# Performance work log

Hardware: AMD Instinct MI355X
Metric: run time of the kernel (lower is better)

The kernel has to match this reference:

```python
import jax, jax.numpy as jnp
import numpy as np

B, T, I, H, FUT = 16384, 50, 6, 128, 30


def setup_inputs() -> dict:
    key = jax.random.key(0)
    ks = jax.random.split(key, 10)
    bound = 1.0 / np.sqrt(H)
    u = lambda k, shape: jax.random.uniform(k, shape, jnp.float32, -bound, bound)
    return {
        "history": jax.random.normal(ks[0], (B, T, I), jnp.float32),
        # GRU weights (PyTorch layout: gates stacked [r, z, n])
        "w_ih": u(ks[1], (3 * H, I)),
        "w_hh": u(ks[2], (3 * H, H)),
        "b_ih": u(ks[3], (3 * H,)),
        "b_hh": u(ks[4], (3 * H,)),
        # MLP head: Linear(H,H) -> ReLU -> Linear(H,I)
        "w1": u(ks[5], (H, H)),
        "b1": u(ks[6], (H,)),
        "w2": u(ks[7], (I, H)),
        "b2": u(ks[8], (I,)),
    }


def _gru_cell(h, x, w_ih, w_hh, b_ih, b_hh):
    # PyTorch GRU cell: gates ordered r, z, n
    gi = x @ w_ih.T + b_ih          # (B, 3H)
    gh = h @ w_hh.T + b_hh          # (B, 3H)
    i_r, i_z, i_n = jnp.split(gi, 3, axis=-1)
    h_r, h_z, h_n = jnp.split(gh, 3, axis=-1)
    r = jax.nn.sigmoid(i_r + h_r)
    z = jax.nn.sigmoid(i_z + h_z)
    n = jnp.tanh(i_n + r * h_n)
    return (1.0 - z) * n + z * h


def reference(history, w_ih, w_hh, b_ih, b_hh, w1, b1, w2, b2):
    # --- encode history: scan GRU over time ---
    h0 = jnp.zeros((history.shape[0], H), history.dtype)

    def enc_step(h, x_t):
        return _gru_cell(h, x_t, w_ih, w_hh, b_ih, b_hh), None

    h_last, _ = jax.lax.scan(enc_step, h0, jnp.swapaxes(history, 0, 1))  # (B, H)

    def head(h):
        return jax.nn.relu(h @ w1.T + b1) @ w2.T + b2  # (B, I)

    def dec_step(carry, _):
        h, x = carry
        h = _gru_cell(h, x, w_ih, w_hh, b_ih, b_hh)
        x = head(h)
        return (h, x), x

    x0 = history[:, -1]  # (B, I)
    _, preds = jax.lax.scan(dec_step, (h_last, x0), None, length=FUT)  # (FUT, B, I)
    return jnp.swapaxes(preds, 0, 1)  # (B, FUT, I)
```

## Files before the change

kernel.cpp:

```cpp
#include <hip/hip_runtime.h>

typedef _Float16 half8 __attribute__((ext_vector_type(8)));
typedef float f32x4 __attribute__((ext_vector_type(4)));

#define ROWS 32
#define HP 136
#define HBUFSZ (ROWS * HP)
#define LOG2E 1.442695041f
#define MFMA(a, b, c) __builtin_amdgcn_mfma_f32_16x16x32_f16((a), (b), (c), 0, 0, 0)

__global__ __launch_bounds__(512, 4)
void traj_gru(const float* __restrict__ history,
              const float* __restrict__ w_ih, const float* __restrict__ w_hh,
              const float* __restrict__ b_ih, const float* __restrict__ b_hh,
              const float* __restrict__ w1, const float* __restrict__ b1,
              const float* __restrict__ w2, const float* __restrict__ b2,
              float* __restrict__ out)
{
    __shared__ __align__(16) _Float16 hbuf[2 * HBUFSZ];
    __shared__ __align__(16) _Float16 xhist[50 * ROWS * 8];
    __shared__ __align__(16) _Float16 xdec[ROWS * 8];
    __shared__ __align__(16) _Float16 a1s[ROWS * HP];
    __shared__ __align__(16) _Float16 w2f[4 * 4 * 16 * 8];

    const int tid  = threadIdx.x;
    const int wave = tid >> 6;
    const int lane = tid & 63;
    const int ln16 = lane & 15;
    const int q    = lane >> 4;
    const int rowbase = blockIdx.x * ROWS;
    const int cbase = wave * 16;

    for (int i = tid; i < 2 * HBUFSZ; i += 512) hbuf[i] = (_Float16)0;
    for (int i = tid; i < 50 * ROWS * 8; i += 512) xhist[i] = (_Float16)0;
    for (int i = tid; i < ROWS * 8; i += 512) xdec[i] = (_Float16)0;
    for (int i = tid; i < 4 * 4 * 16 * 8; i += 512) w2f[i] = (_Float16)0;
    __syncthreads();

    for (int idx = tid; idx < ROWS * 300; idx += 512) {
        int r = idx / 300, rem = idx - r * 300;
        int t = rem / 6, c = rem - t * 6;
        xhist[(t * ROWS + r) * 8 + c] = (_Float16)history[(rowbase + r) * 300 + rem];
    }
    for (int idx = tid; idx < 50 * ROWS; idx += 512)
        xhist[idx * 8 + 6] = (_Float16)1.0f;
    for (int idx = tid; idx < ROWS; idx += 512)
        xdec[idx * 8 + 6] = (_Float16)1.0f;
    for (int idx = tid; idx < 6 * 128; idx += 512) {
        int n = idx >> 7, k = idx & 127;
        int kt = k >> 5, qq = (k >> 3) & 3, j = k & 7;
        w2f[((kt * 4 + qq) * 16 + n) * 8 + j] = (_Float16)w2[n * 128 + k];
    }

    half8 Bh[3][4];
    #pragma unroll
    for (int g = 0; g < 3; ++g) {
        float sc = (g < 2) ? -LOG2E : -2.0f * LOG2E;
        #pragma unroll
        for (int kt = 0; kt < 4; ++kt) {
            int n = g * 128 + cbase + ln16;
            const float* p = w_hh + n * 128 + kt * 32 + q * 8;
            half8 v;
            #pragma unroll
            for (int j = 0; j < 8; ++j) v[j] = (_Float16)(p[j] * sc);
            Bh[g][kt] = v;
        }
    }
    half8 Bi[3];
    #pragma unroll
    for (int g = 0; g < 3; ++g) {
        float sc = (g < 2) ? -LOG2E : -2.0f * LOG2E;
        int n = g * 128 + cbase + ln16;
        half8 v;
        #pragma unroll
        for (int j = 0; j < 8; ++j) v[j] = (_Float16)0.0f;
        if (q == 0) {
            #pragma unroll
            for (int j = 0; j < 6; ++j) v[j] = (_Float16)(w_ih[n * 6 + j] * sc);
            v[6] = (_Float16)((b_ih[n] + (g < 2 ? b_hh[n] : 0.0f)) * sc);
        }
        Bi[g] = v;
    }
    const float bhn = b_hh[256 + cbase + ln16] * (-2.0f * LOG2E);
    half8 Bw1[4];
    #pragma unroll
    for (int kt = 0; kt < 4; ++kt) {
        int n = cbase + ln16;
        const float* p = w1 + n * 128 + kt * 32 + q * 8;
        half8 v;
        #pragma unroll
        for (int j = 0; j < 8; ++j) v[j] = (_Float16)p[j];
        Bw1[kt] = v;
    }
    const float b1r = b1[cbase + ln16];
    const float b2r = (ln16 < 6) ? b2[ln16] : 0.0f;

    float hp[2][4] = {};

    __syncthreads();

    auto gru_step = [&](int p, const _Float16* xp) {
        const _Float16* hb = hbuf + p * HBUFSZ;
        _Float16*       hn = hbuf + (p ^ 1) * HBUFSZ;
        #pragma unroll
        for (int mt = 0; mt < 2; ++mt) {
            const _Float16* rp = hb + (mt * 16 + ln16) * HP + q * 8;
            half8 Ax = {0,0,0,0,0,0,0,0};
            if (q == 0) Ax = *(const half8*)(xp + (mt * 16 + ln16) * 8);
            f32x4 ar = {0,0,0,0}, az = {0,0,0,0}, ah = {0,0,0,0}, an = {0,0,0,0};
            half8 Acur = *(const half8*)(rp);
            #pragma unroll
            for (int kt = 0; kt < 4; ++kt) {
                half8 Anext;
                if (kt < 3) Anext = *(const half8*)(rp + (kt + 1) * 32);
                ar = MFMA(Acur, Bh[0][kt], ar);
                az = MFMA(Acur, Bh[1][kt], az);
                ah = MFMA(Acur, Bh[2][kt], ah);
                Acur = Anext;
            }
            ar = MFMA(Ax, Bi[0], ar);
            az = MFMA(Ax, Bi[1], az);
            an = MFMA(Ax, Bi[2], an);
            _Float16* wp = hn + (mt * 16 + q * 4) * HP + cbase + ln16;
            #pragma unroll
            for (int i = 0; i < 4; ++i) {
                float r = __builtin_amdgcn_rcpf(1.0f + __builtin_amdgcn_exp2f(ar[i]));
                float z = __builtin_amdgcn_rcpf(1.0f + __builtin_amdgcn_exp2f(az[i]));
                float t = an[i] + r * (ah[i] + bhn);
                float n = 2.0f * __builtin_amdgcn_rcpf(1.0f + __builtin_amdgcn_exp2f(t)) - 1.0f;
                float h = n + z * (hp[mt][i] - n);
                hp[mt][i] = h;
                wp[i * HP] = (_Float16)h;
            }
        }
        __syncthreads();
    };

    auto head_step = [&](int f, int p) {
        const _Float16* hb = hbuf + p * HBUFSZ;
        #pragma unroll
        for (int mt = 0; mt < 2; ++mt) {
            const _Float16* rp = hb + (mt * 16 + ln16) * HP + q * 8;
            f32x4 a = {0,0,0,0};
            half8 Acur = *(const half8*)(rp);
            #pragma unroll
            for (int kt = 0; kt < 4; ++kt) {
                half8 Anext;
                if (kt < 3) Anext = *(const half8*)(rp + (kt + 1) * 32);
                a = MFMA(Acur, Bw1[kt], a);
                Acur = Anext;
            }
            _Float16* wp = a1s + (mt * 16 + q * 4) * HP + cbase + ln16;
            #pragma unroll
            for (int i = 0; i < 4; ++i) {
                float v = a[i] + b1r;
                v = v > 0.0f ? v : 0.0f;
                wp[i * HP] = (_Float16)v;
            }
        }
        __syncthreads();
        if (wave < 2) {
            f32x4 o = {0,0,0,0};
            #pragma unroll
            for (int kt = 0; kt < 4; ++kt) {
                half8 Aa = *(const half8*)&a1s[(wave * 16 + ln16) * HP + kt * 32 + q * 8];
                half8 Bw = *(const half8*)&w2f[((kt * 4 + q) * 16 + ln16) * 8];
                o = MFMA(Aa, Bw, o);
            }
            if (ln16 < 6) {
                #pragma unroll
                for (int i = 0; i < 4; ++i) {
                    int row = wave * 16 + q * 4 + i;
                    float v = o[i] + b2r;
                    out[(rowbase + row) * 180 + f * 6 + ln16] = v;
                    xdec[row * 8 + ln16] = (_Float16)v;
                }
            }
        }
        __syncthreads();
    };

    int p = 0;
    #pragma unroll 1
    for (int t = 0; t < 50; ++t) { gru_step(p, xhist + t * ROWS * 8); p ^= 1; }
    #pragma unroll 1
    for (int f = 0; f < 30; ++f) {
        gru_step(p, f == 0 ? xhist + 49 * ROWS * 8 : xdec);
        p ^= 1;
        head_step(f, p);
    }
}

extern "C" void kernel_launch(void* const* d_in, const int* in_sizes, int n_in,
                              void* d_out, int out_size, void* d_ws, size_t ws_size,
                              hipStream_t stream) {
    (void)in_sizes; (void)n_in; (void)d_ws; (void)ws_size; (void)out_size;
    traj_gru<<<dim3(16384 / ROWS), dim3(512), 0, stream>>>(
        (const float*)d_in[0], (const float*)d_in[1], (const float*)d_in[2],
        (const float*)d_in[3], (const float*)d_in[4], (const float*)d_in[5],
        (const float*)d_in[6], (const float*)d_in[7], (const float*)d_in[8],
        (float*)d_out);
}
```

Before: 287.4 us.

## Double rows per block, swizzle LDS layout, pipeline chunks, stage outputs in LDS

Raises rows per block from 32 to 64, so each wave now processes four 16-row chunks per step and the register-held weights and barriers are shared across more rows. Loads and MFMAs for the next chunk are issued before the gate math of the current chunk, giving more overlap inside each wave. The hidden and activation buffers use an XOR swizzle on 32-column blocks to cut LDS bank conflicts. Predictions are staged in LDS, in a buffer that reuses the history area, and written out coalesced at the end. The trade-offs are a much larger LDS footprint, so fewer blocks fit per CU, and the history buffer is no longer zero-initialised, so its padding lane can hold garbage.

```diff
diff --git a/kernel.cpp b/kernel.cpp
--- a/kernel.cpp
+++ b/kernel.cpp
@@ -3,13 +3,14 @@
 typedef _Float16 half8 __attribute__((ext_vector_type(8)));
 typedef float f32x4 __attribute__((ext_vector_type(4)));
 
-#define ROWS 32
+#define ROWS 64
 #define HP 136
 #define HBUFSZ (ROWS * HP)
+#define OP 184
 #define LOG2E 1.442695041f
-#define MFMA(a, b, c) __builtin_amdgcn_mfma_f32_16x16x32_f16((a), (b), (c), 0, 0, 0)
-
-__global__ __launch_bounds__(512, 4)
+#define MFMA(a,b,c) __builtin_amdgcn_mfma_f32_16x16x32_f16((a),(b),(c),0,0,0)
+
+__global__ __launch_bounds__(512, 2)
 void traj_gru(const float* __restrict__ history,
               const float* __restrict__ w_ih, const float* __restrict__ w_hh,
               const float* __restrict__ b_ih, const float* __restrict__ b_hh,
@@ -18,34 +19,36 @@
               float* __restrict__ out)
 {
     __shared__ __align__(16) _Float16 hbuf[2 * HBUFSZ];
-    __shared__ __align__(16) _Float16 xhist[50 * ROWS * 8];
+    __shared__ __align__(16) unsigned char xo_u[50 * ROWS * 16];
     __shared__ __align__(16) _Float16 xdec[ROWS * 8];
     __shared__ __align__(16) _Float16 a1s[ROWS * HP];
     __shared__ __align__(16) _Float16 w2f[4 * 4 * 16 * 8];
+
+    _Float16* xhist = (_Float16*)xo_u;
+    float*    outs  = (float*)xo_u;
 
     const int tid  = threadIdx.x;
     const int wave = tid >> 6;
     const int lane = tid & 63;
     const int ln16 = lane & 15;
     const int q    = lane >> 4;
+    const int sw   = ln16 & 3;
     const int rowbase = blockIdx.x * ROWS;
     const int cbase = wave * 16;
+    const int bblk  = wave >> 1;
+    const int colin = ((wave & 1) << 4) | ln16;
 
     for (int i = tid; i < 2 * HBUFSZ; i += 512) hbuf[i] = (_Float16)0;
-    for (int i = tid; i < 50 * ROWS * 8; i += 512) xhist[i] = (_Float16)0;
     for (int i = tid; i < ROWS * 8; i += 512) xdec[i] = (_Float16)0;
     for (int i = tid; i < 4 * 4 * 16 * 8; i += 512) w2f[i] = (_Float16)0;
     __syncthreads();
-
     for (int idx = tid; idx < ROWS * 300; idx += 512) {
         int r = idx / 300, rem = idx - r * 300;
         int t = rem / 6, c = rem - t * 6;
         xhist[(t * ROWS + r) * 8 + c] = (_Float16)history[(rowbase + r) * 300 + rem];
     }
-    for (int idx = tid; idx < 50 * ROWS; idx += 512)
-        xhist[idx * 8 + 6] = (_Float16)1.0f;
-    for (int idx = tid; idx < ROWS; idx += 512)
-        xdec[idx * 8 + 6] = (_Float16)1.0f;
+    for (int idx = tid; idx < 50 * ROWS; idx += 512) xhist[idx * 8 + 6] = (_Float16)1.0f;
+    for (int idx = tid; idx < ROWS; idx += 512)      xdec[idx * 8 + 6] = (_Float16)1.0f;
     for (int idx = tid; idx < 6 * 128; idx += 512) {
         int n = idx >> 7, k = idx & 127;
         int kt = k >> 5, qq = (k >> 3) & 3, j = k & 7;
@@ -95,42 +98,53 @@
     const float b1r = b1[cbase + ln16];
     const float b2r = (ln16 < 6) ? b2[ln16] : 0.0f;
 
-    float hp[2][4] = {};
+    float hp[4][4] = {};
 
     __syncthreads();
 
     auto gru_step = [&](int p, const _Float16* xp) {
         const _Float16* hb = hbuf + p * HBUFSZ;
         _Float16*       hn = hbuf + (p ^ 1) * HBUFSZ;
-        #pragma unroll
-        for (int mt = 0; mt < 2; ++mt) {
-            const _Float16* rp = hb + (mt * 16 + ln16) * HP + q * 8;
-            half8 Ax = {0,0,0,0,0,0,0,0};
-            if (q == 0) Ax = *(const half8*)(xp + (mt * 16 + ln16) * 8);
-            f32x4 ar = {0,0,0,0}, az = {0,0,0,0}, ah = {0,0,0,0}, an = {0,0,0,0};
-            half8 Acur = *(const half8*)(rp);
+        half8 Ah[2][4], Ax[2];
+        f32x4 ar[2], az[2], ahh[2], an[2];
+
+        auto loadA = [&](int c, int buf) {
+            const _Float16* rp = hb + (c * 16 + ln16) * HP;
+            #pragma unroll
+            for (int kt = 0; kt < 4; ++kt)
+                Ah[buf][kt] = *(const half8*)(rp + ((kt ^ sw) << 5) + q * 8);
+            half8 x = {0,0,0,0,0,0,0,0};
+            if (q == 0) x = *(const half8*)(xp + (c * 16 + ln16) * 8);
+            Ax[buf] = x;
+        };
+        auto mfmas = [&](int buf) {
+            f32x4 r = {0,0,0,0}, z = {0,0,0,0}, hh = {0,0,0,0}, n = {0,0,0,0};
             #pragma unroll
             for (int kt = 0; kt < 4; ++kt) {
-                half8 Anext;
-                if (kt < 3) Anext = *(const half8*)(rp + (kt + 1) * 32);
-                ar = MFMA(Acur, Bh[0][kt], ar);
-                az = MFMA(Acur, Bh[1][kt], az);
-                ah = MFMA(Acur, Bh[2][kt], ah);
-                Acur = Anext;
-            }
-            ar = MFMA(Ax, Bi[0], ar);
-            az = MFMA(Ax, Bi[1], az);
-            an = MFMA(Ax, Bi[2], an);
-            _Float16* wp = hn + (mt * 16 + q * 4) * HP + cbase + ln16;
+                r  = MFMA(Ah[buf][kt], Bh[0][kt], r);
+                z  = MFMA(Ah[buf][kt], Bh[1][kt], z);
+                hh = MFMA(Ah[buf][kt], Bh[2][kt], hh);
+            }
+            r = MFMA(Ax[buf], Bi[0], r);
+            z = MFMA(Ax[buf], Bi[1], z);
+            n = MFMA(Ax[buf], Bi[2], n);
+            ar[buf] = r; az[buf] = z; ahh[buf] = hh; an[buf] = n;
+        };
+
+        loadA(0, 0); mfmas(0);
+        #pragma unroll
+        for (int c = 0; c < 4; ++c) {
+            const int cb = c & 1;
+            if (c < 3) { loadA(c + 1, cb ^ 1); mfmas(cb ^ 1); }
             #pragma unroll
             for (int i = 0; i < 4; ++i) {
-                float r = __builtin_amdgcn_rcpf(1.0f + __builtin_amdgcn_exp2f(ar[i]));
-                float z = __builtin_amdgcn_rcpf(1.0f + __builtin_amdgcn_exp2f(az[i]));
-                float t = an[i] + r * (ah[i] + bhn);
+                float r = __builtin_amdgcn_rcpf(1.0f + __builtin_amdgcn_exp2f(ar[cb][i]));
+                float z = __builtin_amdgcn_rcpf(1.0f + __builtin_amdgcn_exp2f(az[cb][i]));
+                float t = an[cb][i] + r * (ahh[cb][i] + bhn);
                 float n = 2.0f * __builtin_amdgcn_rcpf(1.0f + __builtin_amdgcn_exp2f(t)) - 1.0f;
-                float h = n + z * (hp[mt][i] - n);
-                hp[mt][i] = h;
-                wp[i * HP] = (_Float16)h;
+                float h = n + z * (hp[c][i] - n);
+                hp[c][i] = h;
+                hn[(c * 16 + q * 4 + i) * HP + ((bblk ^ i) << 5) + colin] = (_Float16)h;
             }
         }
         __syncthreads();
@@ -138,32 +152,39 @@
 
     auto head_step = [&](int f, int p) {
         const _Float16* hb = hbuf + p * HBUFSZ;
-        #pragma unroll
-        for (int mt = 0; mt < 2; ++mt) {
-            const _Float16* rp = hb + (mt * 16 + ln16) * HP + q * 8;
+        half8 Ah[2][4];
+        f32x4 aa[2];
+        auto loadA = [&](int c, int buf) {
+            const _Float16* rp = hb + (c * 16 + ln16) * HP;
+            #pragma unroll
+            for (int kt = 0; kt < 4; ++kt)
+                Ah[buf][kt] = *(const half8*)(rp + ((kt ^ sw) << 5) + q * 8);
+        };
+        auto mfh = [&](int buf) {
             f32x4 a = {0,0,0,0};
-            half8 Acur = *(const half8*)(rp);
+            #pragma unroll
+            for (int kt = 0; kt < 4; ++kt) a = MFMA(Ah[buf][kt], Bw1[kt], a);
+            aa[buf] = a;
+        };
+        loadA(0, 0); mfh(0);
+        #pragma unroll
+        for (int c = 0; c < 4; ++c) {
+            const int cb = c & 1;
+            if (c < 3) { loadA(c + 1, cb ^ 1); mfh(cb ^ 1); }
+            #pragma unroll
+            for (int i = 0; i < 4; ++i) {
+                float v = aa[cb][i] + b1r;
+                v = v > 0.0f ? v : 0.0f;
+                a1s[(c * 16 + q * 4 + i) * HP + ((bblk ^ i) << 5) + colin] = (_Float16)v;
+            }
+        }
+        __syncthreads();
+        if (wave < 4) {
+            const _Float16* rp = a1s + (wave * 16 + ln16) * HP;
+            f32x4 o = {0,0,0,0};
             #pragma unroll
             for (int kt = 0; kt < 4; ++kt) {
-                half8 Anext;
-                if (kt < 3) Anext = *(const half8*)(rp + (kt + 1) * 32);
-                a = MFMA(Acur, Bw1[kt], a);
-                Acur = Anext;
-            }
-            _Float16* wp = a1s + (mt * 16 + q * 4) * HP + cbase + ln16;
-            #pragma unroll
-            for (int i = 0; i < 4; ++i) {
-                float v = a[i] + b1r;
-                v = v > 0.0f ? v : 0.0f;
-                wp[i * HP] = (_Float16)v;
-            }
-        }
-        __syncthreads();
-        if (wave < 2) {
-            f32x4 o = {0,0,0,0};
-            #pragma unroll
-            for (int kt = 0; kt < 4; ++kt) {
-                half8 Aa = *(const half8*)&a1s[(wave * 16 + ln16) * HP + kt * 32 + q * 8];
+                half8 Aa = *(const half8*)(rp + ((kt ^ sw) << 5) + q * 8);
                 half8 Bw = *(const half8*)&w2f[((kt * 4 + q) * 16 + ln16) * 8];
                 o = MFMA(Aa, Bw, o);
             }
@@ -172,7 +193,7 @@
                 for (int i = 0; i < 4; ++i) {
                     int row = wave * 16 + q * 4 + i;
                     float v = o[i] + b2r;
-                    out[(rowbase + row) * 180 + f * 6 + ln16] = v;
+                    outs[row * OP + f * 6 + ln16] = v;
                     xdec[row * 8 + ln16] = (_Float16)v;
                 }
             }
@@ -188,6 +209,11 @@
         gru_step(p, f == 0 ? xhist + 49 * ROWS * 8 : xdec);
         p ^= 1;
         head_step(f, p);
+    }
+
+    for (int idx = tid; idx < ROWS * 180; idx += 512) {
+        int r = idx / 180, j = idx - r * 180;
+        out[(rowbase + r) * 180 + j] = outs[r * OP + j];
     }
 }
 
```

Result: no change. 282.0 us (-1.9%).
